# Kernel tuning notes

Hardware: AMD Instinct MI355X
Metric: run time of the kernel (lower is better)

## Reference

```python
import jax, jax.numpy as jnp
from jax import lax
import numpy as np

V, H, L, C, T = 32000, 1024, 256, 32, 64
SOS_TOKEN = 0


def _lstm_cell(h, c, x, Wih, Whh, bih, bhh):
    # h,c,x: [1,H]; Wih,Whh: [4H,H] (torch gate order i,f,g,o)
    g = x @ Wih.T + h @ Whh.T + bih + bhh
    i, f, gg, o = jnp.split(g, 4, axis=-1)
    c = jax.nn.sigmoid(f) * c + jax.nn.sigmoid(i) * jnp.tanh(gg)
    h = jax.nn.sigmoid(o) * jnp.tanh(c)
    return h, c


def setup_inputs() -> dict:
    key = jax.random.key(0)
    ks = jax.random.split(key, 24)
    s = 1.0 / np.sqrt(H)
    n = lambda k, shp, sc: (jax.random.normal(k, shp, dtype=jnp.float32) * sc)
    return {
        "word": jax.random.randint(ks[0], (1, T), 0, V),
        "tense": jax.random.randint(ks[1], (1,), 0, 4),
        "use_teacher_forcing": 1,
        "tense_emb": n(ks[2], (4, C), 0.02),
        "enc_emb": n(ks[3], (V, H), 0.02),
        "enc_Wih": n(ks[4], (4 * H, H), s),
        "enc_Whh": n(ks[5], (4 * H, H), s),
        "enc_bih": n(ks[6], (4 * H,), s),
        "enc_bhh": n(ks[7], (4 * H,), s),
        "W_mean": n(ks[8], (L, H), s),
        "b_mean": n(ks[9], (L,), s),
        "W_var": n(ks[10], (L, H), s),
        "b_var": n(ks[11], (L,), s),
        "W_l2h": n(ks[12], (H, L + C), s),
        "b_l2h": n(ks[13], (H,), s),
        "dec_emb": n(ks[14], (V, H), 0.02),
        "dec_Wih": n(ks[15], (4 * H, H), s),
        "dec_Whh": n(ks[16], (4 * H, H), s),
        "dec_bih": n(ks[17], (4 * H,), s),
        "dec_bhh": n(ks[18], (4 * H,), s),
        "W_out": n(ks[19], (V, H), s),
        "b_out": n(ks[20], (V,), s),
        "eps": jax.random.normal(ks[21], (L,), dtype=jnp.float32),
    }


def reference(word, tense, use_teacher_forcing, tense_emb, enc_emb, enc_Wih,
              enc_Whh, enc_bih, enc_bhh, W_mean, b_mean, W_var, b_var,
              W_l2h, b_l2h, dec_emb, dec_Wih, dec_Whh, dec_bih, dec_bhh,
              W_out, b_out, eps):
    tense_e = tense_emb[tense]                       # [1, C]
    # Encoder: initial hidden = [zeros(H-C) | tense_emb]
    h0 = jnp.concatenate([jnp.zeros((1, H - C), tense_e.dtype), tense_e], axis=-1)
    c0 = jnp.zeros((1, H), tense_e.dtype)
    enc_x = enc_emb[word[0]]                         # [T, H]

    def enc_step(carry, x):
        h, c = _lstm_cell(carry[0], carry[1], x[None], enc_Wih, enc_Whh, enc_bih, enc_bhh)
        return (h, c), None

    (h, _c), _ = lax.scan(enc_step, (h0, c0), enc_x)
    mean = h @ W_mean.T + b_mean                     # [1, L]
    logvar = h @ W_var.T + b_var                     # [1, L]
    latent = mean + eps * jnp.exp(0.5 * logvar)      # reparameterize

    dec_h0 = jnp.concatenate([latent, tense_e], axis=-1) @ W_l2h.T + b_l2h  # [1,H]
    dec_c0 = jnp.zeros((1, H), dec_h0.dtype)

    # teacher forcing: inputs are [SOS, word[0][0], ..., word[0][T-2]]
    dec_in = jnp.concatenate([jnp.full((1,), SOS_TOKEN, word.dtype), word[0, :-1]])
    dec_x = jax.nn.relu(dec_emb[dec_in])             # [T, H]

    def dec_step(carry, x):
        h, c = _lstm_cell(carry[0], carry[1], x[None], dec_Wih, dec_Whh, dec_bih, dec_bhh)
        logits = h @ W_out.T + b_out                 # [1, V]
        return (h, c), jax.nn.log_softmax(logits, axis=-1)[0]

    _, pred_distribution = lax.scan(dec_step, (dec_h0, dec_c0), dec_x)  # [T, V]
    pred_output = jnp.argmax(pred_distribution, axis=1)                 # [T]
    return pred_output, pred_distribution, mean, logvar
```

## Files before the change

kernel.cpp:

```cpp
#include <hip/hip_runtime.h>
#include <math.h>

#define Hd 1024
#define Td 64
#define Vd 32000

static const size_t OFF_GENC  = 131072;
static const size_t OFF_GDEC  = 393216;
static const size_t OFF_BSE   = 655360;
static const size_t OFF_BSD   = 659456;
static const size_t OFF_TEN   = 663552;
static const size_t OFF_HALL  = 663584;
static const size_t OFF_STATS = 729120;
static const size_t OFF_MB    = 730144;

#define MB_H_PAIRS  133120u
#define MB_PAIRS    133376u
#define FLAGB       0x3f800000u

__device__ __forceinline__ float fsigm(float x) {
  return __fdividef(1.f, 1.f + __expf(-x));
}
__device__ __forceinline__ float ftanh(float x) {
  return 1.f - __fdividef(2.f, __expf(2.f * x) + 1.f);
}

__device__ __forceinline__ void st_flag(unsigned long long* p, float v) {
  unsigned long long u = 0x3f80000000000000ull | (unsigned long long)__float_as_uint(v);
  __hip_atomic_store(p, u, __ATOMIC_RELAXED, __HIP_MEMORY_SCOPE_AGENT);
}

__device__ __forceinline__ float4 poll16(const float2* p) {
  float4 a;
  for (;;) {
    asm volatile("global_load_dwordx4 %0, %1, off sc0 sc1\n\ts_waitcnt vmcnt(0)"
                 : "=&v"(a) : "v"(p) : "memory");
    if (__float_as_uint(a.y) == FLAGB && __float_as_uint(a.w) == FLAGB) return a;
  }
}

__device__ __forceinline__ void stage1024(const float2* base, float* dst, int tid) {
  float4 a = poll16(base + 2 * tid);
  ((float2*)dst)[tid] = make_float2(a.x, a.z);
  __syncthreads();
}

__global__ void prep_kernel(const int* __restrict__ tense,
                            const float* __restrict__ tense_emb,
                            const float* __restrict__ enc_bih, const float* __restrict__ enc_bhh,
                            const float* __restrict__ dec_bih, const float* __restrict__ dec_bhh,
                            float* __restrict__ ws) {
  int gid = blockIdx.x * blockDim.x + threadIdx.x;
  int gsz = gridDim.x * blockDim.x;
  int tens = tense[0];
  for (int i = gid; i < 4096; i += gsz) {
    ws[OFF_BSE + i] = enc_bih[i] + enc_bhh[i];
    ws[OFF_BSD + i] = dec_bih[i] + dec_bhh[i];
  }
  for (int i = gid; i < 32; i += gsz) ws[OFF_TEN + i] = tense_emb[tens * 32 + i];
  float2* mb = (float2*)(ws + OFF_MB);
  for (int i = gid; i < (int)MB_PAIRS; i += gsz) {
    float2 v;
    if (i < (int)MB_H_PAIRS && (i >> 10) == 0) {
      int j = i & 1023;
      v.x = (j < Hd - 32) ? 0.f : tense_emb[tens * 32 + (j - (Hd - 32))];
      v.y = 1.0f;
    } else { v.x = 0.f; v.y = 0.f; }
    mb[i] = v;
  }
}

__device__ __forceinline__ void gemm_body(const float* __restrict__ W,
                                          const float* __restrict__ x,
                                          const float* __restrict__ bias,
                                          float* __restrict__ out, int R, int rbase) {
  __shared__ float xs[64][68];
  __shared__ float wsh[64][68];
  const int tid = threadIdx.x;
  const int a = tid >> 4;
  const int b = tid & 15;
  const int sr = tid & 63;
  const int kq = (tid >> 6) << 4;
  float acc[4][4];
#pragma unroll
  for (int i = 0; i < 4; ++i)
#pragma unroll
    for (int q = 0; q < 4; ++q) acc[i][q] = 0.f;

  for (int kc = 0; kc < 1024; kc += 64) {
    const float4* gx = (const float4*)(x + (size_t)sr * 1024 + kc + kq);
    const float4* gw = (const float4*)(W + (size_t)(rbase + sr) * 1024 + kc + kq);
    float4 vx0 = gx[0], vx1 = gx[1], vx2 = gx[2], vx3 = gx[3];
    float4 vw0 = gw[0], vw1 = gw[1], vw2 = gw[2], vw3 = gw[3];
    __syncthreads();
    xs[kq +  0][sr] = vx0.x; xs[kq +  1][sr] = vx0.y; xs[kq +  2][sr] = vx0.z; xs[kq +  3][sr] = vx0.w;
    xs[kq +  4][sr] = vx1.x; xs[kq +  5][sr] = vx1.y; xs[kq +  6][sr] = vx1.z; xs[kq +  7][sr] = vx1.w;
    xs[kq +  8][sr] = vx2.x; xs[kq +  9][sr] = vx2.y; xs[kq + 10][sr] = vx2.z; xs[kq + 11][sr] = vx2.w;
    xs[kq + 12][sr] = vx3.x; xs[kq + 13][sr] = vx3.y; xs[kq + 14][sr] = vx3.z; xs[kq + 15][sr] = vx3.w;
    wsh[kq +  0][sr] = vw0.x; wsh[kq +  1][sr] = vw0.y; wsh[kq +  2][sr] = vw0.z; wsh[kq +  3][sr] = vw0.w;
    wsh[kq +  4][sr] = vw1.x; wsh[kq +  5][sr] = vw1.y; wsh[kq +  6][sr] = vw1.z; wsh[kq +  7][sr] = vw1.w;
    wsh[kq +  8][sr] = vw2.x; wsh[kq +  9][sr] = vw2.y; wsh[kq + 10][sr] = vw2.z; wsh[kq + 11][sr] = vw2.w;
    wsh[kq + 12][sr] = vw3.x; wsh[kq + 13][sr] = vw3.y; wsh[kq + 14][sr] = vw3.z; wsh[kq + 15][sr] = vw3.w;
    __syncthreads();
#pragma unroll 8
    for (int kk = 0; kk < 64; ++kk) {
      float4 xv = *(const float4*)&xs[kk][a * 4];
      float4 wv = *(const float4*)&wsh[kk][b * 4];
      acc[0][0] = fmaf(xv.x, wv.x, acc[0][0]); acc[0][1] = fmaf(xv.x, wv.y, acc[0][1]);
      acc[0][2] = fmaf(xv.x, wv.z, acc[0][2]); acc[0][3] = fmaf(xv.x, wv.w, acc[0][3]);
      acc[1][0] = fmaf(xv.y, wv.x, acc[1][0]); acc[1][1] = fmaf(xv.y, wv.y, acc[1][1]);
      acc[1][2] = fmaf(xv.y, wv.z, acc[1][2]); acc[1][3] = fmaf(xv.y, wv.w, acc[1][3]);
      acc[2][0] = fmaf(xv.z, wv.x, acc[2][0]); acc[2][1] = fmaf(xv.z, wv.y, acc[2][1]);
      acc[2][2] = fmaf(xv.z, wv.z, acc[2][2]); acc[2][3] = fmaf(xv.z, wv.w, acc[2][3]);
      acc[3][0] = fmaf(xv.w, wv.x, acc[3][0]); acc[3][1] = fmaf(xv.w, wv.y, acc[3][1]);
      acc[3][2] = fmaf(xv.w, wv.z, acc[3][2]); acc[3][3] = fmaf(xv.w, wv.w, acc[3][3]);
    }
  }
  const int rb = rbase + b * 4;
  float4 bv = *(const float4*)(bias + rb);
#pragma unroll
  for (int i = 0; i < 4; ++i) {
    int t = a * 4 + i;
    float4 o;
    o.x = acc[i][0] + bv.x; o.y = acc[i][1] + bv.y;
    o.z = acc[i][2] + bv.z; o.w = acc[i][3] + bv.w;
    *(float4*)(out + (size_t)t * R + rb) = o;
  }
}

__device__ __forceinline__ void gemm_gather_body(const float* __restrict__ W,
                                                 const float* __restrict__ emb,
                                                 const int* __restrict__ word, int dec_mode,
                                                 const float* __restrict__ bias,
                                                 float* __restrict__ out, int R, int rbase) {
  __shared__ float xs[64][68];
  __shared__ float wsh[64][68];
  const int tid = threadIdx.x;
  const int a = tid >> 4;
  const int b = tid & 15;
  const int sr = tid & 63;
  const int kq = (tid >> 6) << 4;
  const int tok = dec_mode ? ((sr == 0) ? 0 : word[sr - 1]) : word[sr];
  const float* xrow = emb + (size_t)tok * 1024;
  float acc[4][4];
#pragma unroll
  for (int i = 0; i < 4; ++i)
#pragma unroll
    for (int q = 0; q < 4; ++q) acc[i][q] = 0.f;

  for (int kc = 0; kc < 1024; kc += 64) {
    const float4* gx = (const float4*)(xrow + kc + kq);
    const float4* gw = (const float4*)(W + (size_t)(rbase + sr) * 1024 + kc + kq);
    float4 vx0 = gx[0], vx1 = gx[1], vx2 = gx[2], vx3 = gx[3];
    float4 vw0 = gw[0], vw1 = gw[1], vw2 = gw[2], vw3 = gw[3];
    if (dec_mode) {
      vx0.x = fmaxf(vx0.x, 0.f); vx0.y = fmaxf(vx0.y, 0.f); vx0.z = fmaxf(vx0.z, 0.f); vx0.w = fmaxf(vx0.w, 0.f);
      vx1.x = fmaxf(vx1.x, 0.f); vx1.y = fmaxf(vx1.y, 0.f); vx1.z = fmaxf(vx1.z, 0.f); vx1.w = fmaxf(vx1.w, 0.f);
      vx2.x = fmaxf(vx2.x, 0.f); vx2.y = fmaxf(vx2.y, 0.f); vx2.z = fmaxf(vx2.z, 0.f); vx2.w = fmaxf(vx2.w, 0.f);
      vx3.x = fmaxf(vx3.x, 0.f); vx3.y = fmaxf(vx3.y, 0.f); vx3.z = fmaxf(vx3.z, 0.f); vx3.w = fmaxf(vx3.w, 0.f);
    }
    __syncthreads();
    xs[kq +  0][sr] = vx0.x; xs[kq +  1][sr] = vx0.y; xs[kq +  2][sr] = vx0.z; xs[kq +  3][sr] = vx0.w;
    xs[kq +  4][sr] = vx1.x; xs[kq +  5][sr] = vx1.y; xs[kq +  6][sr] = vx1.z; xs[kq +  7][sr] = vx1.w;
    xs[kq +  8][sr] = vx2.x; xs[kq +  9][sr] = vx2.y; xs[kq + 10][sr] = vx2.z; xs[kq + 11][sr] = vx2.w;
    xs[kq + 12][sr] = vx3.x; xs[kq + 13][sr] = vx3.y; xs[kq + 14][sr] = vx3.z; xs[kq + 15][sr] = vx3.w;
    wsh[kq +  0][sr] = vw0.x; wsh[kq +  1][sr] = vw0.y; wsh[kq +  2][sr] = vw0.z; wsh[kq +  3][sr] = vw0.w;
    wsh[kq +  4][sr] = vw1.x; wsh[kq +  5][sr] = vw1.y; wsh[kq +  6][sr] = vw1.z; wsh[kq +  7][sr] = vw1.w;
    wsh[kq +  8][sr] = vw2.x; wsh[kq +  9][sr] = vw2.y; wsh[kq + 10][sr] = vw2.z; wsh[kq + 11][sr] = vw2.w;
    wsh[kq + 12][sr] = vw3.x; wsh[kq + 13][sr] = vw3.y; wsh[kq + 14][sr] = vw3.z; wsh[kq + 15][sr] = vw3.w;
    __syncthreads();
#pragma unroll 8
    for (int kk = 0; kk < 64; ++kk) {
      float4 xv = *(const float4*)&xs[kk][a * 4];
      float4 wv = *(const float4*)&wsh[kk][b * 4];
      acc[0][0] = fmaf(xv.x, wv.x, acc[0][0]); acc[0][1] = fmaf(xv.x, wv.y, acc[0][1]);
      acc[0][2] = fmaf(xv.x, wv.z, acc[0][2]); acc[0][3] = fmaf(xv.x, wv.w, acc[0][3]);
      acc[1][0] = fmaf(xv.y, wv.x, acc[1][0]); acc[1][1] = fmaf(xv.y, wv.y, acc[1][1]);
      acc[1][2] = fmaf(xv.y, wv.z, acc[1][2]); acc[1][3] = fmaf(xv.y, wv.w, acc[1][3]);
      acc[2][0] = fmaf(xv.z, wv.x, acc[2][0]); acc[2][1] = fmaf(xv.z, wv.y, acc[2][1]);
      acc[2][2] = fmaf(xv.z, wv.z, acc[2][2]); acc[2][3] = fmaf(xv.z, wv.w, acc[2][3]);
      acc[3][0] = fmaf(xv.w, wv.x, acc[3][0]); acc[3][1] = fmaf(xv.w, wv.y, acc[3][1]);
      acc[3][2] = fmaf(xv.w, wv.z, acc[3][2]); acc[3][3] = fmaf(xv.w, wv.w, acc[3][3]);
    }
  }
  const int rb = rbase + b * 4;
  float4 bv = *(const float4*)(bias + rb);
#pragma unroll
  for (int i = 0; i < 4; ++i) {
    int t = a * 4 + i;
    float4 o;
    o.x = acc[i][0] + bv.x; o.y = acc[i][1] + bv.y;
    o.z = acc[i][2] + bv.z; o.w = acc[i][3] + bv.w;
    *(float4*)(out + (size_t)t * R + rb) = o;
  }
}

__global__ __launch_bounds__(256, 2) void gemm_kernel(const float* __restrict__ W,
                                                      const float* __restrict__ x,
                                                      const float* __restrict__ bias,
                                                      float* __restrict__ out, int R) {
  gemm_body(W, x, bias, out, R, blockIdx.x * 64);
}

__global__ __launch_bounds__(256, 2) void gemm_dual_kernel(
    const float* __restrict__ enc_emb, const float* __restrict__ dec_emb,
    const int* __restrict__ word,
    const float* __restrict__ W0, const float* __restrict__ b0, float* __restrict__ o0,
    const float* __restrict__ W1, const float* __restrict__ b1, float* __restrict__ o1) {
  if (blockIdx.x < 64)
    gemm_gather_body(W0, enc_emb, word, 0, b0, o0, 4096, blockIdx.x * 64);
  else
    gemm_gather_body(W1, dec_emb, word, 1, b1, o1, 4096, (blockIdx.x - 64) * 64);
}

__device__ __forceinline__ void gload16(const float* base, float* d) {
  asm volatile(
      "global_load_dword %0, %16, off\n\t"
      "global_load_dword %1, %16, off offset:256\n\t"
      "global_load_dword %2, %16, off offset:512\n\t"
      "global_load_dword %3, %16, off offset:768\n\t"
      "global_load_dword %4, %16, off offset:1024\n\t"
      "global_load_dword %5, %16, off offset:1280\n\t"
      "global_load_dword %6, %16, off offset:1536\n\t"
      "global_load_dword %7, %16, off offset:1792\n\t"
      "global_load_dword %8, %16, off offset:2048\n\t"
      "global_load_dword %9, %16, off offset:2304\n\t"
      "global_load_dword %10, %16, off offset:2560\n\t"
      "global_load_dword %11, %16, off offset:2816\n\t"
      "global_load_dword %12, %16, off offset:3072\n\t"
      "global_load_dword %13, %16, off offset:3328\n\t"
      "global_load_dword %14, %16, off offset:3584\n\t"
      "global_load_dword %15, %16, off offset:3840\n\t"
      "s_waitcnt vmcnt(0)"
      : "=&v"(d[0]), "=&v"(d[1]), "=&v"(d[2]), "=&v"(d[3]),
        "=&v"(d[4]), "=&v"(d[5]), "=&v"(d[6]), "=&v"(d[7]),
        "=&v"(d[8]), "=&v"(d[9]), "=&v"(d[10]), "=&v"(d[11]),
        "=&v"(d[12]), "=&v"(d[13]), "=&v"(d[14]), "=&v"(d[15])
      : "v"(base));
}

__global__ __launch_bounds__(512, 2) void seq_kernel(
    const float* __restrict__ enc_Whh, const float* __restrict__ dec_Whh,
    const float* __restrict__ W_mean, const float* __restrict__ b_mean,
    const float* __restrict__ W_var, const float* __restrict__ b_var,
    const float* __restrict__ W_l2h, const float* __restrict__ b_l2h,
    const float* __restrict__ eps, float* __restrict__ ws, float* __restrict__ dout) {
  __shared__ float hsbuf[2][Hd];
  __shared__ float lat[288];
  const int tid = threadIdx.x;
  const int lane = tid & 63;
  const int wid = tid >> 6;
  const int j = blockIdx.x * 8 + wid;

  float2* mb = (float2*)(ws + OFF_MB);
  unsigned long long* mbq = (unsigned long long*)(ws + OFF_MB);
  const float* Genc = ws + OFF_GENC;
  const float* Gdec = ws + OFF_GDEC;
  float* h_all = ws + OFF_HALL;

  float we[4][16], wd[4][16];
#pragma unroll
  for (int r = 0; r < 4; ++r) {
    const size_t ro = (size_t)(r * Hd + j) * Hd + lane;
    gload16(enc_Whh + ro, we[r]);
    gload16(dec_Whh + ro, wd[r]);
  }

  float c_reg = 0.f;
  float gb0 = Genc[j], gb1 = Genc[1024 + j], gb2 = Genc[2048 + j], gb3 = Genc[3072 + j];
  for (int t = 0; t < Td; ++t) {
    stage1024(mb + (size_t)t * 1024, hsbuf[t & 1], tid);
    const float* hs = hsbuf[t & 1];
    float p0 = 0.f, p1 = 0.f, p2 = 0.f, p3 = 0.f;
#pragma unroll
    for (int i = 0; i < 16; ++i) {
      float hv = hs[lane + 64 * i];
      p0 = fmaf(we[0][i], hv, p0);
      p1 = fmaf(we[1][i], hv, p1);
      p2 = fmaf(we[2][i], hv, p2);
      p3 = fmaf(we[3][i], hv, p3);
    }
#pragma unroll
    for (int off = 32; off; off >>= 1) {
      p0 += __shfl_xor(p0, off, 64); p1 += __shfl_xor(p1, off, 64);
      p2 += __shfl_xor(p2, off, 64); p3 += __shfl_xor(p3, off, 64);
    }
    float gi = gb0 + p0, gf = gb1 + p1, gg = gb2 + p2, go = gb3 + p3;
    c_reg = fsigm(gf) * c_reg + fsigm(gi) * ftanh(gg);
    float hval = fsigm(go) * ftanh(c_reg);
    if (lane == 0) st_flag(mbq + (size_t)(t + 1) * 1024 + j, hval);
    if (t + 1 < Td) {
      gb0 = Genc[(t + 1) * 4096 + j];
      gb1 = Genc[(t + 1) * 4096 + 1024 + j];
      gb2 = Genc[(t + 1) * 4096 + 2048 + j];
      gb3 = Genc[(t + 1) * 4096 + 3072 + j];
    }
  }

  if (j < 256) {
    stage1024(mb + (size_t)Td * 1024, hsbuf[0], tid);
    const float* hs = hsbuf[0];
    const float* Wm = W_mean + (size_t)j * Hd;
    const float* Wv = W_var + (size_t)j * Hd;
    float pm = 0.f, pv = 0.f;
#pragma unroll
    for (int i = 0; i < 16; ++i) {
      float hv = hs[lane + 64 * i];
      pm = fmaf(Wm[lane + 64 * i], hv, pm);
      pv = fmaf(Wv[lane + 64 * i], hv, pv);
    }
#pragma unroll
    for (int off = 32; off; off >>= 1) {
      pm += __shfl_xor(pm, off, 64); pv += __shfl_xor(pv, off, 64);
    }
    if (lane == 0) {
      float m = pm + b_mean[j];
      float lv = pv + b_var[j];
      dout[2048064 + j] = m;
      dout[2048320 + j] = lv;
      float latv = m + eps[j] * __expf(0.5f * lv);
      st_flag(mbq + MB_H_PAIRS + j, latv);
    }
  }

  if (tid < 128) {
    float4 a = poll16(mb + MB_H_PAIRS + 2 * tid);
    lat[2 * tid] = a.x; lat[2 * tid + 1] = a.z;
  } else if (tid < 160) {
    lat[256 + (tid - 128)] = ws[OFF_TEN + (tid - 128)];
  }
  __syncthreads();

  {
    const float* Wr = W_l2h + (size_t)j * 288;
    float p = fmaf(Wr[lane], lat[lane], 0.f);
    p = fmaf(Wr[lane + 64], lat[lane + 64], p);
    p = fmaf(Wr[lane + 128], lat[lane + 128], p);
    p = fmaf(Wr[lane + 192], lat[lane + 192], p);
    if (lane < 32) p = fmaf(Wr[lane + 256], lat[lane + 256], p);
#pragma unroll
    for (int off = 32; off; off >>= 1) p += __shfl_xor(p, off, 64);
    if (lane == 0) st_flag(mbq + (size_t)65 * 1024 + j, p + b_l2h[j]);
  }
  __syncthreads();

  c_reg = 0.f;
  gb0 = Gdec[j]; gb1 = Gdec[1024 + j]; gb2 = Gdec[2048 + j]; gb3 = Gdec[3072 + j];
  for (int t = 0; t < Td; ++t) {
    stage1024(mb + (size_t)(65 + t) * 1024, hsbuf[t & 1], tid);
    const float* hs = hsbuf[t & 1];
    float p0 = 0.f, p1 = 0.f, p2 = 0.f, p3 = 0.f;
#pragma unroll
    for (int i = 0; i < 16; ++i) {
      float hv = hs[lane + 64 * i];
      p0 = fmaf(wd[0][i], hv, p0);
      p1 = fmaf(wd[1][i], hv, p1);
      p2 = fmaf(wd[2][i], hv, p2);
      p3 = fmaf(wd[3][i], hv, p3);
    }
#pragma unroll
    for (int off = 32; off; off >>= 1) {
      p0 += __shfl_xor(p0, off, 64); p1 += __shfl_xor(p1, off, 64);
      p2 += __shfl_xor(p2, off, 64); p3 += __shfl_xor(p3, off, 64);
    }
    float gi = gb0 + p0, gf = gb1 + p1, gg = gb2 + p2, go = gb3 + p3;
    c_reg = fsigm(gf) * c_reg + fsigm(gi) * ftanh(gg);
    float hval = fsigm(go) * ftanh(c_reg);
    if (lane == 0) {
      if (t + 1 < Td) st_flag(mbq + (size_t)(66 + t) * 1024 + j, hval);
      h_all[(size_t)t * Hd + j] = hval;
    }
    if (t + 1 < Td) {
      gb0 = Gdec[(t + 1) * 4096 + j];
      gb1 = Gdec[(t + 1) * 4096 + 1024 + j];
      gb2 = Gdec[(t + 1) * 4096 + 2048 + j];
      gb3 = Gdec[(t + 1) * 4096 + 3072 + j];
    }
  }
}

__global__ __launch_bounds__(256) void lstats_kernel(const float* __restrict__ logits,
                                                     float* __restrict__ sd) {
  const int blk = blockIdx.x, t = blk >> 2, q = blk & 3, tid = threadIdx.x;
  const float* row = logits + (size_t)t * Vd + q * 8000;
  __shared__ float sm[256];
  __shared__ int si[256];
  float m = -INFINITY; int mi = 0x7fffffff;
  for (int v = tid; v < 8000; v += 256) {
    float x = row[v];
    if (x > m) { m = x; mi = v; }
  }
  sm[tid] = m; si[tid] = mi;
  __syncthreads();
  for (int s = 128; s > 0; s >>= 1) {
    if (tid < s) {
      float om = sm[tid + s]; int oi = si[tid + s];
      if (om > sm[tid] || (om == sm[tid] && oi < si[tid])) { sm[tid] = om; si[tid] = oi; }
    }
    __syncthreads();
  }
  float rm = sm[0]; int ri = si[0];
  __syncthreads();
  float s = 0.f;
  for (int v = tid; v < 8000; v += 256) s += __expf(row[v] - rm);
  sm[tid] = s;
  __syncthreads();
  for (int st = 128; st > 0; st >>= 1) {
    if (tid < st) sm[tid] += sm[tid + st];
    __syncthreads();
  }
  if (tid == 0) {
    sd[blk * 4 + 0] = rm;
    sd[blk * 4 + 1] = (float)(ri + q * 8000);
    sd[blk * 4 + 2] = sm[0];
  }
}

__global__ __launch_bounds__(256) void lfin_kernel(float* __restrict__ out,
                                                   const float* __restrict__ sd) {
  const int blk = blockIdx.x, t = blk >> 2, q = blk & 3, tid = threadIdx.x;
  float M = -INFINITY;
#pragma unroll
  for (int k = 0; k < 4; ++k) M = fmaxf(M, sd[t * 16 + k * 4]);
  float S = 0.f;
#pragma unroll
  for (int k = 0; k < 4; ++k) S += sd[t * 16 + k * 4 + 2] * __expf(sd[t * 16 + k * 4] - M);
  float corr = M + logf(S);
  float4* r4 = (float4*)(out + 64 + (size_t)t * Vd + q * 8000);
  for (int i = tid; i < 2000; i += 256) {
    float4 v = r4[i];
    v.x -= corr; v.y -= corr; v.z -= corr; v.w -= corr;
    r4[i] = v;
  }
  if (q == 0 && tid == 0) {
    float bm = -INFINITY; int bi = 0;
#pragma unroll
    for (int k = 0; k < 4; ++k) {
      float m = sd[t * 16 + k * 4];
      if (m > bm) { bm = m; bi = (int)sd[t * 16 + k * 4 + 1]; }
    }
    out[t] = (float)bi;
  }
}

extern "C" void kernel_launch(void* const* d_in, const int* in_sizes, int n_in,
                              void* d_out, int out_size, void* d_ws, size_t ws_size,
                              hipStream_t stream) {
  (void)in_sizes; (void)n_in; (void)out_size; (void)ws_size;
  const int* word       = (const int*)d_in[0];
  const int* tense      = (const int*)d_in[1];
  const float* tense_emb = (const float*)d_in[3];
  const float* enc_emb   = (const float*)d_in[4];
  const float* enc_Wih   = (const float*)d_in[5];
  const float* enc_Whh   = (const float*)d_in[6];
  const float* enc_bih   = (const float*)d_in[7];
  const float* enc_bhh   = (const float*)d_in[8];
  const float* W_mean    = (const float*)d_in[9];
  const float* b_mean    = (const float*)d_in[10];
  const float* W_var     = (const float*)d_in[11];
  const float* b_var     = (const float*)d_in[12];
  const float* W_l2h     = (const float*)d_in[13];
  const float* b_l2h     = (const float*)d_in[14];
  const float* dec_emb   = (const float*)d_in[15];
  const float* dec_Wih   = (const float*)d_in[16];
  const float* dec_Whh   = (const float*)d_in[17];
  const float* dec_bih   = (const float*)d_in[18];
  const float* dec_bhh   = (const float*)d_in[19];
  const float* W_out     = (const float*)d_in[20];
  const float* b_out     = (const float*)d_in[21];
  const float* eps       = (const float*)d_in[22];
  float* out = (float*)d_out;
  float* ws  = (float*)d_ws;

  prep_kernel<<<256, 256, 0, stream>>>(tense, tense_emb, enc_bih, enc_bhh,
                                       dec_bih, dec_bhh, ws);
  gemm_dual_kernel<<<128, 256, 0, stream>>>(enc_emb, dec_emb, word,
                                            enc_Wih, ws + OFF_BSE, ws + OFF_GENC,
                                            dec_Wih, ws + OFF_BSD, ws + OFF_GDEC);
  seq_kernel<<<128, 512, 0, stream>>>(enc_Whh, dec_Whh, W_mean, b_mean, W_var, b_var,
                                      W_l2h, b_l2h, eps, ws, out);
  gemm_kernel<<<500, 256, 0, stream>>>(W_out, ws + OFF_HALL, b_out, out + 64, 32000);
  lstats_kernel<<<256, 256, 0, stream>>>(out + 64, ws + OFF_STATS);
  lfin_kernel<<<256, 256, 0, stream>>>(out, ws + OFF_STATS);
}
```

Baseline: 520.6 us.

## Fuse output projection and softmax stats into the recurrent kernel as consumer blocks

Merges the sequential LSTM kernel, the vocab-projection GEMM and the log-softmax stats kernel into one persistent launch. Blocks 0-127 run the recurrence while 125 extra blocks poll the decoder hidden states in chunks of 16 steps and compute logits plus per-256-column max and sum-exp as each chunk becomes ready. This overlaps the W_out GEMM with the serial decoder and removes the separate stats pass over the logits. The cost is a 125-way reduction in the final kernel, spin-polling blocks that need co-residency with the recurrent blocks, and a GEMM tile shape that may be less efficient.

```diff
diff --git a/kernel.cpp b/kernel.cpp
--- a/kernel.cpp
+++ b/kernel.cpp
@@ -10,9 +10,8 @@
 static const size_t OFF_BSE   = 655360;
 static const size_t OFF_BSD   = 659456;
 static const size_t OFF_TEN   = 663552;
-static const size_t OFF_HALL  = 663584;
-static const size_t OFF_STATS = 729120;
 static const size_t OFF_MB    = 730144;
+static const size_t OFF_ST2   = 1000000;
 
 #define MB_H_PAIRS  133120u
 #define MB_PAIRS    133376u
@@ -70,10 +69,11 @@
   }
 }
 
-__device__ __forceinline__ void gemm_body(const float* __restrict__ W,
-                                          const float* __restrict__ x,
-                                          const float* __restrict__ bias,
-                                          float* __restrict__ out, int R, int rbase) {
+__device__ __forceinline__ void gemm_gather_body(const float* __restrict__ W,
+                                                 const float* __restrict__ emb,
+                                                 const int* __restrict__ word, int dec_mode,
+                                                 const float* __restrict__ bias,
+                                                 float* __restrict__ out, int R, int rbase) {
   __shared__ float xs[64][68];
   __shared__ float wsh[64][68];
   const int tid = threadIdx.x;
@@ -81,6 +81,8 @@
   const int b = tid & 15;
   const int sr = tid & 63;
   const int kq = (tid >> 6) << 4;
+  const int tok = dec_mode ? ((sr == 0) ? 0 : word[sr - 1]) : word[sr];
+  const float* xrow = emb + (size_t)tok * 1024;
   float acc[4][4];
 #pragma unroll
   for (int i = 0; i < 4; ++i)
@@ -88,10 +90,16 @@
     for (int q = 0; q < 4; ++q) acc[i][q] = 0.f;
 
   for (int kc = 0; kc < 1024; kc += 64) {
-    const float4* gx = (const float4*)(x + (size_t)sr * 1024 + kc + kq);
+    const float4* gx = (const float4*)(xrow + kc + kq);
     const float4* gw = (const float4*)(W + (size_t)(rbase + sr) * 1024 + kc + kq);
     float4 vx0 = gx[0], vx1 = gx[1], vx2 = gx[2], vx3 = gx[3];
     float4 vw0 = gw[0], vw1 = gw[1], vw2 = gw[2], vw3 = gw[3];
+    if (dec_mode) {
+      vx0.x = fmaxf(vx0.x, 0.f); vx0.y = fmaxf(vx0.y, 0.f); vx0.z = fmaxf(vx0.z, 0.f); vx0.w = fmaxf(vx0.w, 0.f);
+      vx1.x = fmaxf(vx1.x, 0.f); vx1.y = fmaxf(vx1.y, 0.f); vx1.z = fmaxf(vx1.z, 0.f); vx1.w = fmaxf(vx1.w, 0.f);
+      vx2.x = fmaxf(vx2.x, 0.f); vx2.y = fmaxf(vx2.y, 0.f); vx2.z = fmaxf(vx2.z, 0.f); vx2.w = fmaxf(vx2.w, 0.f);
+      vx3.x = fmaxf(vx3.x, 0.f); vx3.y = fmaxf(vx3.y, 0.f); vx3.z = fmaxf(vx3.z, 0.f); vx3.w = fmaxf(vx3.w, 0.f);
+    }
     __syncthreads();
     xs[kq +  0][sr] = vx0.x; xs[kq +  1][sr] = vx0.y; xs[kq +  2][sr] = vx0.z; xs[kq +  3][sr] = vx0.w;
     xs[kq +  4][sr] = vx1.x; xs[kq +  5][sr] = vx1.y; xs[kq +  6][sr] = vx1.z; xs[kq +  7][sr] = vx1.w;
@@ -126,80 +134,6 @@
     o.z = acc[i][2] + bv.z; o.w = acc[i][3] + bv.w;
     *(float4*)(out + (size_t)t * R + rb) = o;
   }
-}
-
-__device__ __forceinline__ void gemm_gather_body(const float* __restrict__ W,
-                                                 const float* __restrict__ emb,
-                                                 const int* __restrict__ word, int dec_mode,
-                                                 const float* __restrict__ bias,
-                                                 float* __restrict__ out, int R, int rbase) {
-  __shared__ float xs[64][68];
-  __shared__ float wsh[64][68];
-  const int tid = threadIdx.x;
-  const int a = tid >> 4;
-  const int b = tid & 15;
-  const int sr = tid & 63;
-  const int kq = (tid >> 6) << 4;
-  const int tok = dec_mode ? ((sr == 0) ? 0 : word[sr - 1]) : word[sr];
-  const float* xrow = emb + (size_t)tok * 1024;
-  float acc[4][4];
-#pragma unroll
-  for (int i = 0; i < 4; ++i)
-#pragma unroll
-    for (int q = 0; q < 4; ++q) acc[i][q] = 0.f;
-
-  for (int kc = 0; kc < 1024; kc += 64) {
-    const float4* gx = (const float4*)(xrow + kc + kq);
-    const float4* gw = (const float4*)(W + (size_t)(rbase + sr) * 1024 + kc + kq);
-    float4 vx0 = gx[0], vx1 = gx[1], vx2 = gx[2], vx3 = gx[3];
-    float4 vw0 = gw[0], vw1 = gw[1], vw2 = gw[2], vw3 = gw[3];
-    if (dec_mode) {
-      vx0.x = fmaxf(vx0.x, 0.f); vx0.y = fmaxf(vx0.y, 0.f); vx0.z = fmaxf(vx0.z, 0.f); vx0.w = fmaxf(vx0.w, 0.f);
-      vx1.x = fmaxf(vx1.x, 0.f); vx1.y = fmaxf(vx1.y, 0.f); vx1.z = fmaxf(vx1.z, 0.f); vx1.w = fmaxf(vx1.w, 0.f);
-      vx2.x = fmaxf(vx2.x, 0.f); vx2.y = fmaxf(vx2.y, 0.f); vx2.z = fmaxf(vx2.z, 0.f); vx2.w = fmaxf(vx2.w, 0.f);
-      vx3.x = fmaxf(vx3.x, 0.f); vx3.y = fmaxf(vx3.y, 0.f); vx3.z = fmaxf(vx3.z, 0.f); vx3.w = fmaxf(vx3.w, 0.f);
-    }
-    __syncthreads();
-    xs[kq +  0][sr] = vx0.x; xs[kq +  1][sr] = vx0.y; xs[kq +  2][sr] = vx0.z; xs[kq +  3][sr] = vx0.w;
-    xs[kq +  4][sr] = vx1.x; xs[kq +  5][sr] = vx1.y; xs[kq +  6][sr] = vx1.z; xs[kq +  7][sr] = vx1.w;
-    xs[kq +  8][sr] = vx2.x; xs[kq +  9][sr] = vx2.y; xs[kq + 10][sr] = vx2.z; xs[kq + 11][sr] = vx2.w;
-    xs[kq + 12][sr] = vx3.x; xs[kq + 13][sr] = vx3.y; xs[kq + 14][sr] = vx3.z; xs[kq + 15][sr] = vx3.w;
-    wsh[kq +  0][sr] = vw0.x; wsh[kq +  1][sr] = vw0.y; wsh[kq +  2][sr] = vw0.z; wsh[kq +  3][sr] = vw0.w;
-    wsh[kq +  4][sr] = vw1.x; wsh[kq +  5][sr] = vw1.y; wsh[kq +  6][sr] = vw1.z; wsh[kq +  7][sr] = vw1.w;
-    wsh[kq +  8][sr] = vw2.x; wsh[kq +  9][sr] = vw2.y; wsh[kq + 10][sr] = vw2.z; wsh[kq + 11][sr] = vw2.w;
-    wsh[kq + 12][sr] = vw3.x; wsh[kq + 13][sr] = vw3.y; wsh[kq + 14][sr] = vw3.z; wsh[kq + 15][sr] = vw3.w;
-    __syncthreads();
-#pragma unroll 8
-    for (int kk = 0; kk < 64; ++kk) {
-      float4 xv = *(const float4*)&xs[kk][a * 4];
-      float4 wv = *(const float4*)&wsh[kk][b * 4];
-      acc[0][0] = fmaf(xv.x, wv.x, acc[0][0]); acc[0][1] = fmaf(xv.x, wv.y, acc[0][1]);
-      acc[0][2] = fmaf(xv.x, wv.z, acc[0][2]); acc[0][3] = fmaf(xv.x, wv.w, acc[0][3]);
-      acc[1][0] = fmaf(xv.y, wv.x, acc[1][0]); acc[1][1] = fmaf(xv.y, wv.y, acc[1][1]);
-      acc[1][2] = fmaf(xv.y, wv.z, acc[1][2]); acc[1][3] = fmaf(xv.y, wv.w, acc[1][3]);
-      acc[2][0] = fmaf(xv.z, wv.x, acc[2][0]); acc[2][1] = fmaf(xv.z, wv.y, acc[2][1]);
-      acc[2][2] = fmaf(xv.z, wv.z, acc[2][2]); acc[2][3] = fmaf(xv.z, wv.w, acc[2][3]);
-      acc[3][0] = fmaf(xv.w, wv.x, acc[3][0]); acc[3][1] = fmaf(xv.w, wv.y, acc[3][1]);
-      acc[3][2] = fmaf(xv.w, wv.z, acc[3][2]); acc[3][3] = fmaf(xv.w, wv.w, acc[3][3]);
-    }
-  }
-  const int rb = rbase + b * 4;
-  float4 bv = *(const float4*)(bias + rb);
-#pragma unroll
-  for (int i = 0; i < 4; ++i) {
-    int t = a * 4 + i;
-    float4 o;
-    o.x = acc[i][0] + bv.x; o.y = acc[i][1] + bv.y;
-    o.z = acc[i][2] + bv.z; o.w = acc[i][3] + bv.w;
-    *(float4*)(out + (size_t)t * R + rb) = o;
-  }
-}
-
-__global__ __launch_bounds__(256, 2) void gemm_kernel(const float* __restrict__ W,
-                                                      const float* __restrict__ x,
-                                                      const float* __restrict__ bias,
-                                                      float* __restrict__ out, int R) {
-  gemm_body(W, x, bias, out, R, blockIdx.x * 64);
 }
 
 __global__ __launch_bounds__(256, 2) void gemm_dual_kernel(
@@ -239,180 +173,244 @@
       : "v"(base));
 }
 
-__global__ __launch_bounds__(512, 2) void seq_kernel(
+__global__ __launch_bounds__(512, 2) void mega_kernel(
     const float* __restrict__ enc_Whh, const float* __restrict__ dec_Whh,
     const float* __restrict__ W_mean, const float* __restrict__ b_mean,
     const float* __restrict__ W_var, const float* __restrict__ b_var,
     const float* __restrict__ W_l2h, const float* __restrict__ b_l2h,
-    const float* __restrict__ eps, float* __restrict__ ws, float* __restrict__ dout) {
-  __shared__ float hsbuf[2][Hd];
-  __shared__ float lat[288];
+    const float* __restrict__ eps, float* __restrict__ ws, float* __restrict__ dout,
+    const float* __restrict__ W_out, const float* __restrict__ b_out) {
+  __shared__ float smem[35072];
   const int tid = threadIdx.x;
   const int lane = tid & 63;
-  const int wid = tid >> 6;
-  const int j = blockIdx.x * 8 + wid;
-
   float2* mb = (float2*)(ws + OFF_MB);
   unsigned long long* mbq = (unsigned long long*)(ws + OFF_MB);
-  const float* Genc = ws + OFF_GENC;
-  const float* Gdec = ws + OFF_GDEC;
-  float* h_all = ws + OFF_HALL;
-
-  float we[4][16], wd[4][16];
-#pragma unroll
-  for (int r = 0; r < 4; ++r) {
-    const size_t ro = (size_t)(r * Hd + j) * Hd + lane;
-    gload16(enc_Whh + ro, we[r]);
-    gload16(dec_Whh + ro, wd[r]);
-  }
-
-  float c_reg = 0.f;
-  float gb0 = Genc[j], gb1 = Genc[1024 + j], gb2 = Genc[2048 + j], gb3 = Genc[3072 + j];
-  for (int t = 0; t < Td; ++t) {
-    stage1024(mb + (size_t)t * 1024, hsbuf[t & 1], tid);
-    const float* hs = hsbuf[t & 1];
-    float p0 = 0.f, p1 = 0.f, p2 = 0.f, p3 = 0.f;
-#pragma unroll
-    for (int i = 0; i < 16; ++i) {
-      float hv = hs[lane + 64 * i];
-      p0 = fmaf(we[0][i], hv, p0);
-      p1 = fmaf(we[1][i], hv, p1);
-      p2 = fmaf(we[2][i], hv, p2);
-      p3 = fmaf(we[3][i], hv, p3);
-    }
-#pragma unroll
-    for (int off = 32; off; off >>= 1) {
-      p0 += __shfl_xor(p0, off, 64); p1 += __shfl_xor(p1, off, 64);
-      p2 += __shfl_xor(p2, off, 64); p3 += __shfl_xor(p3, off, 64);
-    }
-    float gi = gb0 + p0, gf = gb1 + p1, gg = gb2 + p2, go = gb3 + p3;
-    c_reg = fsigm(gf) * c_reg + fsigm(gi) * ftanh(gg);
-    float hval = fsigm(go) * ftanh(c_reg);
-    if (lane == 0) st_flag(mbq + (size_t)(t + 1) * 1024 + j, hval);
-    if (t + 1 < Td) {
-      gb0 = Genc[(t + 1) * 4096 + j];
-      gb1 = Genc[(t + 1) * 4096 + 1024 + j];
-      gb2 = Genc[(t + 1) * 4096 + 2048 + j];
-      gb3 = Genc[(t + 1) * 4096 + 3072 + j];
-    }
-  }
-
-  if (j < 256) {
-    stage1024(mb + (size_t)Td * 1024, hsbuf[0], tid);
-    const float* hs = hsbuf[0];
-    const float* Wm = W_mean + (size_t)j * Hd;
-    const float* Wv = W_var + (size_t)j * Hd;
-    float pm = 0.f, pv = 0.f;
-#pragma unroll
-    for (int i = 0; i < 16; ++i) {
-      float hv = hs[lane + 64 * i];
-      pm = fmaf(Wm[lane + 64 * i], hv, pm);
-      pv = fmaf(Wv[lane + 64 * i], hv, pv);
-    }
-#pragma unroll
-    for (int off = 32; off; off >>= 1) {
-      pm += __shfl_xor(pm, off, 64); pv += __shfl_xor(pv, off, 64);
-    }
-    if (lane == 0) {
-      float m = pm + b_mean[j];
-      float lv = pv + b_var[j];
-      dout[2048064 + j] = m;
-      dout[2048320 + j] = lv;
-      float latv = m + eps[j] * __expf(0.5f * lv);
-      st_flag(mbq + MB_H_PAIRS + j, latv);
-    }
-  }
-
-  if (tid < 128) {
-    float4 a = poll16(mb + MB_H_PAIRS + 2 * tid);
-    lat[2 * tid] = a.x; lat[2 * tid + 1] = a.z;
-  } else if (tid < 160) {
-    lat[256 + (tid - 128)] = ws[OFF_TEN + (tid - 128)];
-  }
-  __syncthreads();
-
-  {
-    const float* Wr = W_l2h + (size_t)j * 288;
-    float p = fmaf(Wr[lane], lat[lane], 0.f);
-    p = fmaf(Wr[lane + 64], lat[lane + 64], p);
-    p = fmaf(Wr[lane + 128], lat[lane + 128], p);
-    p = fmaf(Wr[lane + 192], lat[lane + 192], p);
-    if (lane < 32) p = fmaf(Wr[lane + 256], lat[lane + 256], p);
-#pragma unroll
-    for (int off = 32; off; off >>= 1) p += __shfl_xor(p, off, 64);
-    if (lane == 0) st_flag(mbq + (size_t)65 * 1024 + j, p + b_l2h[j]);
-  }
-  __syncthreads();
-
-  c_reg = 0.f;
-  gb0 = Gdec[j]; gb1 = Gdec[1024 + j]; gb2 = Gdec[2048 + j]; gb3 = Gdec[3072 + j];
-  for (int t = 0; t < Td; ++t) {
-    stage1024(mb + (size_t)(65 + t) * 1024, hsbuf[t & 1], tid);
-    const float* hs = hsbuf[t & 1];
-    float p0 = 0.f, p1 = 0.f, p2 = 0.f, p3 = 0.f;
-#pragma unroll
-    for (int i = 0; i < 16; ++i) {
-      float hv = hs[lane + 64 * i];
-      p0 = fmaf(wd[0][i], hv, p0);
-      p1 = fmaf(wd[1][i], hv, p1);
-      p2 = fmaf(wd[2][i], hv, p2);
-      p3 = fmaf(wd[3][i], hv, p3);
-    }
-#pragma unroll
-    for (int off = 32; off; off >>= 1) {
-      p0 += __shfl_xor(p0, off, 64); p1 += __shfl_xor(p1, off, 64);
-      p2 += __shfl_xor(p2, off, 64); p3 += __shfl_xor(p3, off, 64);
-    }
-    float gi = gb0 + p0, gf = gb1 + p1, gg = gb2 + p2, go = gb3 + p3;
-    c_reg = fsigm(gf) * c_reg + fsigm(gi) * ftanh(gg);
-    float hval = fsigm(go) * ftanh(c_reg);
-    if (lane == 0) {
-      if (t + 1 < Td) st_flag(mbq + (size_t)(66 + t) * 1024 + j, hval);
-      h_all[(size_t)t * Hd + j] = hval;
-    }
-    if (t + 1 < Td) {
-      gb0 = Gdec[(t + 1) * 4096 + j];
-      gb1 = Gdec[(t + 1) * 4096 + 1024 + j];
-      gb2 = Gdec[(t + 1) * 4096 + 2048 + j];
-      gb3 = Gdec[(t + 1) * 4096 + 3072 + j];
-    }
-  }
-}
-
-__global__ __launch_bounds__(256) void lstats_kernel(const float* __restrict__ logits,
-                                                     float* __restrict__ sd) {
-  const int blk = blockIdx.x, t = blk >> 2, q = blk & 3, tid = threadIdx.x;
-  const float* row = logits + (size_t)t * Vd + q * 8000;
-  __shared__ float sm[256];
-  __shared__ int si[256];
-  float m = -INFINITY; int mi = 0x7fffffff;
-  for (int v = tid; v < 8000; v += 256) {
-    float x = row[v];
-    if (x > m) { m = x; mi = v; }
-  }
-  sm[tid] = m; si[tid] = mi;
-  __syncthreads();
-  for (int s = 128; s > 0; s >>= 1) {
-    if (tid < s) {
-      float om = sm[tid + s]; int oi = si[tid + s];
-      if (om > sm[tid] || (om == sm[tid] && oi < si[tid])) { sm[tid] = om; si[tid] = oi; }
+
+  if (blockIdx.x < 128) {
+    float* hsbuf0 = smem;
+    float* hsbuf1 = smem + 1024;
+    float* lat    = smem + 2048;
+    const int wid = tid >> 6;
+    const int j = blockIdx.x * 8 + wid;
+    const float* Genc = ws + OFF_GENC;
+    const float* Gdec = ws + OFF_GDEC;
+
+    float we[4][16], wd[4][16];
+#pragma unroll
+    for (int r = 0; r < 4; ++r) {
+      const size_t ro = (size_t)(r * Hd + j) * Hd + lane;
+      gload16(enc_Whh + ro, we[r]);
+      gload16(dec_Whh + ro, wd[r]);
+    }
+
+    float c_reg = 0.f;
+    float gb0 = Genc[j], gb1 = Genc[1024 + j], gb2 = Genc[2048 + j], gb3 = Genc[3072 + j];
+    for (int t = 0; t < Td; ++t) {
+      float* hsb = (t & 1) ? hsbuf1 : hsbuf0;
+      stage1024(mb + (size_t)t * 1024, hsb, tid);
+      const float* hs = hsb;
+      float p0 = 0.f, p1 = 0.f, p2 = 0.f, p3 = 0.f;
+#pragma unroll
+      for (int i = 0; i < 16; ++i) {
+        float hv = hs[lane + 64 * i];
+        p0 = fmaf(we[0][i], hv, p0);
+        p1 = fmaf(we[1][i], hv, p1);
+        p2 = fmaf(we[2][i], hv, p2);
+        p3 = fmaf(we[3][i], hv, p3);
+      }
+#pragma unroll
+      for (int off = 32; off; off >>= 1) {
+        p0 += __shfl_xor(p0, off, 64); p1 += __shfl_xor(p1, off, 64);
+        p2 += __shfl_xor(p2, off, 64); p3 += __shfl_xor(p3, off, 64);
+      }
+      float gi = gb0 + p0, gf = gb1 + p1, gg = gb2 + p2, go = gb3 + p3;
+      c_reg = fsigm(gf) * c_reg + fsigm(gi) * ftanh(gg);
+      float hval = fsigm(go) * ftanh(c_reg);
+      if (lane == 0) st_flag(mbq + (size_t)(t + 1) * 1024 + j, hval);
+      if (t + 1 < Td) {
+        gb0 = Genc[(t + 1) * 4096 + j];
+        gb1 = Genc[(t + 1) * 4096 + 1024 + j];
+        gb2 = Genc[(t + 1) * 4096 + 2048 + j];
+        gb3 = Genc[(t + 1) * 4096 + 3072 + j];
+      }
+    }
+
+    if (j < 256) {
+      stage1024(mb + (size_t)Td * 1024, hsbuf0, tid);
+      const float* hs = hsbuf0;
+      const float* Wm = W_mean + (size_t)j * Hd;
+      const float* Wv = W_var + (size_t)j * Hd;
+      float pm = 0.f, pv = 0.f;
+#pragma unroll
+      for (int i = 0; i < 16; ++i) {
+        float hv = hs[lane + 64 * i];
+        pm = fmaf(Wm[lane + 64 * i], hv, pm);
+        pv = fmaf(Wv[lane + 64 * i], hv, pv);
+      }
+#pragma unroll
+      for (int off = 32; off; off >>= 1) {
+        pm += __shfl_xor(pm, off, 64); pv += __shfl_xor(pv, off, 64);
+      }
+      if (lane == 0) {
+        float m = pm + b_mean[j];
+        float lv = pv + b_var[j];
+        dout[2048064 + j] = m;
+        dout[2048320 + j] = lv;
+        float latv = m + eps[j] * __expf(0.5f * lv);
+        st_flag(mbq + MB_H_PAIRS + j, latv);
+      }
+    }
+
+    if (tid < 128) {
+      float4 a = poll16(mb + MB_H_PAIRS + 2 * tid);
+      lat[2 * tid] = a.x; lat[2 * tid + 1] = a.z;
+    } else if (tid < 160) {
+      lat[256 + (tid - 128)] = ws[OFF_TEN + (tid - 128)];
     }
     __syncthreads();
-  }
-  float rm = sm[0]; int ri = si[0];
-  __syncthreads();
-  float s = 0.f;
-  for (int v = tid; v < 8000; v += 256) s += __expf(row[v] - rm);
-  sm[tid] = s;
-  __syncthreads();
-  for (int st = 128; st > 0; st >>= 1) {
-    if (tid < st) sm[tid] += sm[tid + st];
+
+    {
+      const float* Wr = W_l2h + (size_t)j * 288;
+      float p = fmaf(Wr[lane], lat[lane], 0.f);
+      p = fmaf(Wr[lane + 64], lat[lane + 64], p);
+      p = fmaf(Wr[lane + 128], lat[lane + 128], p);
+      p = fmaf(Wr[lane + 192], lat[lane + 192], p);
+      if (lane < 32) p = fmaf(Wr[lane + 256], lat[lane + 256], p);
+#pragma unroll
+      for (int off = 32; off; off >>= 1) p += __shfl_xor(p, off, 64);
+      if (lane == 0) st_flag(mbq + (size_t)65 * 1024 + j, p + b_l2h[j]);
+    }
     __syncthreads();
-  }
-  if (tid == 0) {
-    sd[blk * 4 + 0] = rm;
-    sd[blk * 4 + 1] = (float)(ri + q * 8000);
-    sd[blk * 4 + 2] = sm[0];
+
+    c_reg = 0.f;
+    gb0 = Gdec[j]; gb1 = Gdec[1024 + j]; gb2 = Gdec[2048 + j]; gb3 = Gdec[3072 + j];
+    for (int t = 0; t < Td; ++t) {
+      float* hsb = (t & 1) ? hsbuf1 : hsbuf0;
+      stage1024(mb + (size_t)(65 + t) * 1024, hsb, tid);
+      const float* hs = hsb;
+      float p0 = 0.f, p1 = 0.f, p2 = 0.f, p3 = 0.f;
+#pragma unroll
+      for (int i = 0; i < 16; ++i) {
+        float hv = hs[lane + 64 * i];
+        p0 = fmaf(wd[0][i], hv, p0);
+        p1 = fmaf(wd[1][i], hv, p1);
+        p2 = fmaf(wd[2][i], hv, p2);
+        p3 = fmaf(wd[3][i], hv, p3);
+      }
+#pragma unroll
+      for (int off = 32; off; off >>= 1) {
+        p0 += __shfl_xor(p0, off, 64); p1 += __shfl_xor(p1, off, 64);
+        p2 += __shfl_xor(p2, off, 64); p3 += __shfl_xor(p3, off, 64);
+      }
+      float gi = gb0 + p0, gf = gb1 + p1, gg = gb2 + p2, go = gb3 + p3;
+      c_reg = fsigm(gf) * c_reg + fsigm(gi) * ftanh(gg);
+      float hval = fsigm(go) * ftanh(c_reg);
+      if (lane == 0) st_flag(mbq + (size_t)(66 + t) * 1024 + j, hval);
+      if (t + 1 < Td) {
+        gb0 = Gdec[(t + 1) * 4096 + j];
+        gb1 = Gdec[(t + 1) * 4096 + 1024 + j];
+        gb2 = Gdec[(t + 1) * 4096 + 2048 + j];
+        gb3 = Gdec[(t + 1) * 4096 + 3072 + j];
+      }
+    }
+  } else if (blockIdx.x < 253) {
+    const int wb = blockIdx.x - 128;
+    const int rbase = wb * 256;
+    const int a = tid >> 6;
+    float* sd = ws + OFF_ST2;
+    float* out64 = dout + 64;
+
+    for (int c = 0; c < 4; ++c) {
+      if (tid == 0) {
+        const float2* sp = mb + (size_t)(66 + c * 16 + 15) * 1024;
+        for (;;) {
+          float4 s;
+          asm volatile("global_load_dwordx4 %0, %1, off sc0 sc1\n\ts_waitcnt vmcnt(0)"
+                       : "=&v"(s) : "v"(sp) : "memory");
+          if (__float_as_uint(s.y) == FLAGB && __float_as_uint(s.w) == FLAGB) break;
+          __builtin_amdgcn_s_sleep(32);
+        }
+      }
+      __syncthreads();
+      for (int rr = 0; rr < 16; ++rr) {
+        float4 aa = poll16(mb + (size_t)(66 + c * 16 + rr) * 1024 + 2 * tid);
+        smem[(2 * tid) * 18 + rr] = aa.x;
+        smem[(2 * tid + 1) * 18 + rr] = aa.z;
+      }
+      __syncthreads();
+
+      float acc[2][4];
+#pragma unroll
+      for (int i = 0; i < 2; ++i)
+#pragma unroll
+        for (int q = 0; q < 4; ++q) acc[i][q] = 0.f;
+
+      const int rr2 = tid >> 1;
+      const int kh = (tid & 1) * 32;
+      for (int kc = 0; kc < 1024; kc += 64) {
+        const float4* gw = (const float4*)(W_out + (size_t)(rbase + rr2) * 1024 + kc + kh);
+        float4 w0 = gw[0], w1 = gw[1], w2 = gw[2], w3 = gw[3];
+        float4 w4 = gw[4], w5 = gw[5], w6 = gw[6], w7 = gw[7];
+        __syncthreads();
+        float* wp = smem + 18432;
+        wp[(kh + 0) * 260 + rr2] = w0.x; wp[(kh + 1) * 260 + rr2] = w0.y;
+        wp[(kh + 2) * 260 + rr2] = w0.z; wp[(kh + 3) * 260 + rr2] = w0.w;
+        wp[(kh + 4) * 260 + rr2] = w1.x; wp[(kh + 5) * 260 + rr2] = w1.y;
+        wp[(kh + 6) * 260 + rr2] = w1.z; wp[(kh + 7) * 260 + rr2] = w1.w;
+        wp[(kh + 8) * 260 + rr2] = w2.x; wp[(kh + 9) * 260 + rr2] = w2.y;
+        wp[(kh + 10) * 260 + rr2] = w2.z; wp[(kh + 11) * 260 + rr2] = w2.w;
+        wp[(kh + 12) * 260 + rr2] = w3.x; wp[(kh + 13) * 260 + rr2] = w3.y;
+        wp[(kh + 14) * 260 + rr2] = w3.z; wp[(kh + 15) * 260 + rr2] = w3.w;
+        wp[(kh + 16) * 260 + rr2] = w4.x; wp[(kh + 17) * 260 + rr2] = w4.y;
+        wp[(kh + 18) * 260 + rr2] = w4.z; wp[(kh + 19) * 260 + rr2] = w4.w;
+        wp[(kh + 20) * 260 + rr2] = w5.x; wp[(kh + 21) * 260 + rr2] = w5.y;
+        wp[(kh + 22) * 260 + rr2] = w5.z; wp[(kh + 23) * 260 + rr2] = w5.w;
+        wp[(kh + 24) * 260 + rr2] = w6.x; wp[(kh + 25) * 260 + rr2] = w6.y;
+        wp[(kh + 26) * 260 + rr2] = w6.z; wp[(kh + 27) * 260 + rr2] = w6.w;
+        wp[(kh + 28) * 260 + rr2] = w7.x; wp[(kh + 29) * 260 + rr2] = w7.y;
+        wp[(kh + 30) * 260 + rr2] = w7.z; wp[(kh + 31) * 260 + rr2] = w7.w;
+        __syncthreads();
+#pragma unroll 8
+        for (int kk = 0; kk < 64; ++kk) {
+          float2 xv = *(const float2*)&smem[(kc + kk) * 18 + 2 * a];
+          float4 wv = *(const float4*)&smem[18432 + kk * 260 + 4 * lane];
+          acc[0][0] = fmaf(xv.x, wv.x, acc[0][0]); acc[0][1] = fmaf(xv.x, wv.y, acc[0][1]);
+          acc[0][2] = fmaf(xv.x, wv.z, acc[0][2]); acc[0][3] = fmaf(xv.x, wv.w, acc[0][3]);
+          acc[1][0] = fmaf(xv.y, wv.x, acc[1][0]); acc[1][1] = fmaf(xv.y, wv.y, acc[1][1]);
+          acc[1][2] = fmaf(xv.y, wv.z, acc[1][2]); acc[1][3] = fmaf(xv.y, wv.w, acc[1][3]);
+        }
+      }
+      __syncthreads();
+
+      const int r0 = rbase + 4 * lane;
+      float4 bo = *(const float4*)(b_out + r0);
+#pragma unroll
+      for (int i = 0; i < 2; ++i) {
+        const int t = c * 16 + 2 * a + i;
+        float4 o;
+        o.x = acc[i][0] + bo.x; o.y = acc[i][1] + bo.y;
+        o.z = acc[i][2] + bo.z; o.w = acc[i][3] + bo.w;
+        *(float4*)(out64 + (size_t)t * Vd + r0) = o;
+        float m = o.x; int mi = r0;
+        if (o.y > m) { m = o.y; mi = r0 + 1; }
+        if (o.z > m) { m = o.z; mi = r0 + 2; }
+        if (o.w > m) { m = o.w; mi = r0 + 3; }
+#pragma unroll
+        for (int off = 32; off; off >>= 1) {
+          float om = __shfl_xor(m, off, 64);
+          int oi = __shfl_xor(mi, off, 64);
+          if (om > m || (om == m && oi < mi)) { m = om; mi = oi; }
+        }
+        float s = __expf(o.x - m) + __expf(o.y - m) + __expf(o.z - m) + __expf(o.w - m);
+#pragma unroll
+        for (int off = 32; off; off >>= 1) s += __shfl_xor(s, off, 64);
+        if (lane == 0) {
+          sd[(size_t)(t * 125 + wb) * 4 + 0] = m;
+          sd[(size_t)(t * 125 + wb) * 4 + 1] = (float)mi;
+          sd[(size_t)(t * 125 + wb) * 4 + 2] = s;
+        }
+      }
+    }
   }
 }
 
@@ -420,11 +418,10 @@
                                                    const float* __restrict__ sd) {
   const int blk = blockIdx.x, t = blk >> 2, q = blk & 3, tid = threadIdx.x;
   float M = -INFINITY;
-#pragma unroll
-  for (int k = 0; k < 4; ++k) M = fmaxf(M, sd[t * 16 + k * 4]);
+  for (int k = 0; k < 125; ++k) M = fmaxf(M, sd[(size_t)(t * 125 + k) * 4]);
   float S = 0.f;
-#pragma unroll
-  for (int k = 0; k < 4; ++k) S += sd[t * 16 + k * 4 + 2] * __expf(sd[t * 16 + k * 4] - M);
+  for (int k = 0; k < 125; ++k)
+    S += sd[(size_t)(t * 125 + k) * 4 + 2] * __expf(sd[(size_t)(t * 125 + k) * 4] - M);
   float corr = M + logf(S);
   float4* r4 = (float4*)(out + 64 + (size_t)t * Vd + q * 8000);
   for (int i = tid; i < 2000; i += 256) {
@@ -434,10 +431,9 @@
   }
   if (q == 0 && tid == 0) {
     float bm = -INFINITY; int bi = 0;
-#pragma unroll
-    for (int k = 0; k < 4; ++k) {
-      float m = sd[t * 16 + k * 4];
-      if (m > bm) { bm = m; bi = (int)sd[t * 16 + k * 4 + 1]; }
+    for (int k = 0; k < 125; ++k) {
+      float m = sd[(size_t)(t * 125 + k) * 4];
+      if (m > bm) { bm = m; bi = (int)sd[(size_t)(t * 125 + k) * 4 + 1]; }
     }
     out[t] = (float)bi;
   }
@@ -477,9 +473,7 @@
   gemm_dual_kernel<<<128, 256, 0, stream>>>(enc_emb, dec_emb, word,
                                             enc_Wih, ws + OFF_BSE, ws + OFF_GENC,
                                             dec_Wih, ws + OFF_BSD, ws + OFF_GDEC);
-  seq_kernel<<<128, 512, 0, stream>>>(enc_Whh, dec_Whh, W_mean, b_mean, W_var, b_var,
-                                      W_l2h, b_l2h, eps, ws, out);
-  gemm_kernel<<<500, 256, 0, stream>>>(W_out, ws + OFF_HALL, b_out, out + 64, 32000);
-  lstats_kernel<<<256, 256, 0, stream>>>(out + 64, ws + OFF_STATS);
-  lfin_kernel<<<256, 256, 0, stream>>>(out, ws + OFF_STATS);
-}
+  mega_kernel<<<253, 512, 0, stream>>>(enc_Whh, dec_Whh, W_mean, b_mean, W_var, b_var,
+                                       W_l2h, b_l2h, eps, ws, out, W_out, b_out);
+  lfin_kernel<<<256, 256, 0, stream>>>(out, ws + OFF_ST2);
+}
```

After: 639.2 us. +22.8%, slower.
